# Optimization experiments

Measured on AMD Instinct MI355X. Metric: run time of the kernel, lower is better.

Reference implementation:

```python
import jax, jax.numpy as jnp
import numpy as np
from jax import lax

COEF = 0.97  # rnn.weight_hh_l0; weight_ih_l0 == 1.0


def setup_inputs() -> dict:
    key = jax.random.key(0)
    B, C, T = 128, 1, 262144
    x = jax.random.normal(key, (B, C, T), dtype=jnp.float32)
    return {"input": x}


def reference(input) -> jnp.ndarray:
    # torch.nn.RNN(1,1,1,bias=False) with weight_ih=1, weight_hh=COEF and
    # default nonlinearity='tanh':  h[t] = tanh(x[t] + COEF * h[t-1])
    x = input[:, 0, :]                     # [B, T]
    B = x.shape[0]

    def step(h, x_t):                      # h: [B], x_t: [B]
        h = jnp.tanh(x_t + COEF * h)
        return h, h

    h0 = jnp.zeros((B,), dtype=x.dtype)
    _, ys = lax.scan(step, h0, x.T)        # ys: [T, B]
    return ys.T[:, None, :]                # [B, 1, T]
```

## Files before the change

kernel.cpp:

```cpp
#include <hip/hip_runtime.h>


#define BB 128
#define TT 262144
#define CH 64
#define SPW 64
#define NBLK (BB * (TT / CH) / SPW)

typedef float f32x4 __attribute__((ext_vector_type(4)));

__global__ __launch_bounds__(64) void ipe_kernel(const float* __restrict__ x,
                                                 float* __restrict__ y) {
    const int lane = threadIdx.x;
    const int bid = (blockIdx.x & 7) * (NBLK >> 3) + (blockIdx.x >> 3);
    const int row = bid >> 6;
    const int g   = bid & 63;
    const size_t rowBase = (size_t)row * TT;
    const long   tileT0  = (long)g * (SPW * CH) - CH;

    __shared__ float tile[65 * 64];

    const int h4 = lane >> 4;
    const int t4 = lane & 15;

    f32x4 pf[17];
    #pragma unroll
    for (int m = 0; m < 16; ++m) {
        const long T = tileT0 + (long)(m * 64 + lane) * 4;
        if (T >= 0) pf[m] = *reinterpret_cast<const f32x4*>(x + rowBase + T);
        else        pf[m] = (f32x4){0.f, 0.f, 0.f, 0.f};
    }
    if (lane < 16) {
        const long T = tileT0 + (long)(16 * 64 + lane) * 4;
        pf[16] = *reinterpret_cast<const f32x4*>(x + rowBase + T);
    }

    #pragma unroll
    for (int m = 0; m < 16; ++m) {
        const int span = 4 * m + h4;
        *reinterpret_cast<f32x4*>(&tile[span * 64 + 4 * (t4 ^ (span & 15))]) = pf[m];
    }
    if (lane < 16) {
        *reinterpret_cast<f32x4*>(&tile[64 * 64 + 4 * lane]) = pf[16];
    }
    asm volatile("" ::: "memory");

    const float C2 = 2.885390081777926815f;
    const float K2 = 0.97f * C2;
    float h = 0.f;
    float xv[64];

    #pragma unroll
    for (int e = 0; e < 16; ++e) {
        f32x4 v = *reinterpret_cast<const f32x4*>(
            &tile[lane * 64 + 4 * (e ^ (lane & 15))]);
        xv[4 * e + 0] = v.x; xv[4 * e + 1] = v.y;
        xv[4 * e + 2] = v.z; xv[4 * e + 3] = v.w;
    }
    #pragma unroll
    for (int k = 0; k < 64; ++k) {
        float z2 = fmaf(K2, h, xv[k] * C2);
        float ez = __builtin_amdgcn_exp2f(z2);
        float rc = __builtin_amdgcn_rcpf(ez + 1.0f);
        h = fmaf(-2.0f, rc, 1.0f);
    }

    const int sp1 = lane + 1;
    #pragma unroll
    for (int e = 0; e < 16; ++e) {
        f32x4 v = *reinterpret_cast<const f32x4*>(
            &tile[sp1 * 64 + 4 * (e ^ (sp1 & 15))]);
        xv[4 * e + 0] = v.x; xv[4 * e + 1] = v.y;
        xv[4 * e + 2] = v.z; xv[4 * e + 3] = v.w;
    }
    #pragma unroll
    for (int k = 0; k < 64; ++k) {
        float z2 = fmaf(K2, h, xv[k] * C2);
        float ez = __builtin_amdgcn_exp2f(z2);
        float rc = __builtin_amdgcn_rcpf(ez + 1.0f);
        h = fmaf(-2.0f, rc, 1.0f);
        xv[k] = h;
    }

    asm volatile("" ::: "memory");
    #pragma unroll
    for (int e = 0; e < 16; ++e) {
        f32x4 v;
        v.x = xv[4 * e + 0]; v.y = xv[4 * e + 1];
        v.z = xv[4 * e + 2]; v.w = xv[4 * e + 3];
        *reinterpret_cast<f32x4*>(&tile[sp1 * 64 + 4 * (e ^ (sp1 & 15))]) = v;
    }
    asm volatile("" ::: "memory");

    const long outT0 = tileT0 + CH;
    #pragma unroll
    for (int m = 0; m < 16; ++m) {
        const int span = 1 + 4 * m + h4;
        f32x4 v = *reinterpret_cast<const f32x4*>(
            &tile[span * 64 + 4 * (t4 ^ (span & 15))]);
        *reinterpret_cast<f32x4*>(y + rowBase + outT0 + (long)(m * 64 + lane) * 4) = v;
    }
}

extern "C" void kernel_launch(void* const* d_in, const int* in_sizes, int n_in,
                              void* d_out, int out_size, void* d_ws, size_t ws_size,
                              hipStream_t stream) {
    const float* x = (const float*)d_in[0];
    float* y = (float*)d_out;
    ipe_kernel<<<dim3(NBLK), dim3(64), 0, stream>>>(x, y);
}
```

Before: 46.84 us.

## Shrink per-lane chunk to 32 with 64-step warmup window, two waves per block

Each lane now handles 32 outputs instead of 64. Before those, it runs a 64-step warmup recurrence over the preceding inputs (its previous two chunks) so the tanh recurrence converges, replacing the earlier 64-step warmup plus 64-step output layout. Blocks now hold two independent 64-lane waves, each with its own smaller LDS tile and a new XOR swizzle. The aim is to cut the serial dependency chain per lane from 128 to 96 steps, at the cost of a higher warmup-to-output ratio and more total transcendental work. Accuracy now relies on the 0.97 decay over 64 steps being enough, as before.

```diff
diff --git a/kernel.cpp b/kernel.cpp
--- a/kernel.cpp
+++ b/kernel.cpp
@@ -3,78 +3,91 @@
 
 #define BB 128
 #define TT 262144
-#define CH 64
-#define SPW 64
-#define NBLK (BB * (TT / CH) / SPW)
+#define CHL 32
+#define WW 64
+#define WPR 128
+#define NBLK ((BB * WPR) / 2)
 
 typedef float f32x4 __attribute__((ext_vector_type(4)));
 
-__global__ __launch_bounds__(64) void ipe_kernel(const float* __restrict__ x,
-                                                 float* __restrict__ y) {
-    const int lane = threadIdx.x;
-    const int bid = (blockIdx.x & 7) * (NBLK >> 3) + (blockIdx.x >> 3);
-    const int row = bid >> 6;
-    const int g   = bid & 63;
+__device__ __forceinline__ int swq(int q) { return q ^ ((q >> 3) & 7); }
+
+__global__ __launch_bounds__(128) void ipe_kernel(const float* __restrict__ x,
+                                                  float* __restrict__ y) {
+    const int lane = threadIdx.x & 63;
+    const int wv   = threadIdx.x >> 6;
+    const int bid  = (blockIdx.x & 7) * (NBLK >> 3) + (blockIdx.x >> 3);
+    const int w    = bid * 2 + wv;
+    const int row  = w >> 7;
+    const int g    = w & (WPR - 1);
     const size_t rowBase = (size_t)row * TT;
-    const long   tileT0  = (long)g * (SPW * CH) - CH;
+    const long   t0 = (long)g * (64 * CHL);
 
-    __shared__ float tile[65 * 64];
+    __shared__ float tile_all[2][528 * 4];
+    float* tile = tile_all[wv];
 
-    const int h4 = lane >> 4;
-    const int t4 = lane & 15;
-
-    f32x4 pf[17];
+    f32x4 pf[8], ph;
     #pragma unroll
-    for (int m = 0; m < 16; ++m) {
-        const long T = tileT0 + (long)(m * 64 + lane) * 4;
-        if (T >= 0) pf[m] = *reinterpret_cast<const f32x4*>(x + rowBase + T);
-        else        pf[m] = (f32x4){0.f, 0.f, 0.f, 0.f};
-    }
+    for (int m = 0; m < 8; ++m)
+        pf[m] = *reinterpret_cast<const f32x4*>(x + rowBase + t0 + 256 * m + 4 * lane);
     if (lane < 16) {
-        const long T = tileT0 + (long)(16 * 64 + lane) * 4;
-        pf[16] = *reinterpret_cast<const f32x4*>(x + rowBase + T);
+        const long T = t0 - WW + 4 * lane;
+        if (T >= 0) ph = *reinterpret_cast<const f32x4*>(x + rowBase + T);
+        else        ph = (f32x4){0.f, 0.f, 0.f, 0.f};
     }
 
     #pragma unroll
-    for (int m = 0; m < 16; ++m) {
-        const int span = 4 * m + h4;
-        *reinterpret_cast<f32x4*>(&tile[span * 64 + 4 * (t4 ^ (span & 15))]) = pf[m];
+    for (int m = 0; m < 8; ++m)
+        *reinterpret_cast<f32x4*>(&tile[4 * swq(16 + 64 * m + lane)]) = pf[m];
+    if (lane < 16)
+        *reinterpret_cast<f32x4*>(&tile[4 * swq(lane)]) = ph;
+    asm volatile("" ::: "memory");
+
+    float xv[32];
+    #pragma unroll
+    for (int t = 0; t < 8; ++t) {
+        f32x4 v = *reinterpret_cast<const f32x4*>(&tile[4 * swq(8 * lane + t)]);
+        xv[4 * t + 0] = v.x; xv[4 * t + 1] = v.y;
+        xv[4 * t + 2] = v.z; xv[4 * t + 3] = v.w;
     }
-    if (lane < 16) {
-        *reinterpret_cast<f32x4*>(&tile[64 * 64 + 4 * lane]) = pf[16];
-    }
-    asm volatile("" ::: "memory");
+    #pragma unroll
+    for (int t = 0; t < 8; ++t)
+        pf[t] = *reinterpret_cast<const f32x4*>(&tile[4 * swq(8 * lane + 8 + t)]);
 
     const float C2 = 2.885390081777926815f;
     const float K2 = 0.97f * C2;
     float h = 0.f;
-    float xv[64];
 
     #pragma unroll
-    for (int e = 0; e < 16; ++e) {
-        f32x4 v = *reinterpret_cast<const f32x4*>(
-            &tile[lane * 64 + 4 * (e ^ (lane & 15))]);
-        xv[4 * e + 0] = v.x; xv[4 * e + 1] = v.y;
-        xv[4 * e + 2] = v.z; xv[4 * e + 3] = v.w;
-    }
-    #pragma unroll
-    for (int k = 0; k < 64; ++k) {
+    for (int k = 0; k < 32; ++k) {
         float z2 = fmaf(K2, h, xv[k] * C2);
         float ez = __builtin_amdgcn_exp2f(z2);
         float rc = __builtin_amdgcn_rcpf(ez + 1.0f);
         h = fmaf(-2.0f, rc, 1.0f);
     }
 
-    const int sp1 = lane + 1;
     #pragma unroll
-    for (int e = 0; e < 16; ++e) {
-        f32x4 v = *reinterpret_cast<const f32x4*>(
-            &tile[sp1 * 64 + 4 * (e ^ (sp1 & 15))]);
-        xv[4 * e + 0] = v.x; xv[4 * e + 1] = v.y;
-        xv[4 * e + 2] = v.z; xv[4 * e + 3] = v.w;
+    for (int t = 0; t < 8; ++t) {
+        f32x4 v = *reinterpret_cast<const f32x4*>(&tile[4 * swq(16 + 8 * lane + t)]);
+        xv[4 * t + 0] = v.x; xv[4 * t + 1] = v.y;
+        xv[4 * t + 2] = v.z; xv[4 * t + 3] = v.w;
     }
+
     #pragma unroll
-    for (int k = 0; k < 64; ++k) {
+    for (int t = 0; t < 8; ++t) {
+        float z2, ez, rc;
+        z2 = fmaf(K2, h, pf[t].x * C2); ez = __builtin_amdgcn_exp2f(z2);
+        rc = __builtin_amdgcn_rcpf(ez + 1.0f); h = fmaf(-2.0f, rc, 1.0f);
+        z2 = fmaf(K2, h, pf[t].y * C2); ez = __builtin_amdgcn_exp2f(z2);
+        rc = __builtin_amdgcn_rcpf(ez + 1.0f); h = fmaf(-2.0f, rc, 1.0f);
+        z2 = fmaf(K2, h, pf[t].z * C2); ez = __builtin_amdgcn_exp2f(z2);
+        rc = __builtin_amdgcn_rcpf(ez + 1.0f); h = fmaf(-2.0f, rc, 1.0f);
+        z2 = fmaf(K2, h, pf[t].w * C2); ez = __builtin_amdgcn_exp2f(z2);
+        rc = __builtin_amdgcn_rcpf(ez + 1.0f); h = fmaf(-2.0f, rc, 1.0f);
+    }
+
+    #pragma unroll
+    for (int k = 0; k < 32; ++k) {
         float z2 = fmaf(K2, h, xv[k] * C2);
         float ez = __builtin_amdgcn_exp2f(z2);
         float rc = __builtin_amdgcn_rcpf(ez + 1.0f);
@@ -84,21 +97,18 @@
 
     asm volatile("" ::: "memory");
     #pragma unroll
-    for (int e = 0; e < 16; ++e) {
+    for (int t = 0; t < 8; ++t) {
         f32x4 v;
-        v.x = xv[4 * e + 0]; v.y = xv[4 * e + 1];
-        v.z = xv[4 * e + 2]; v.w = xv[4 * e + 3];
-        *reinterpret_cast<f32x4*>(&tile[sp1 * 64 + 4 * (e ^ (sp1 & 15))]) = v;
+        v.x = xv[4 * t + 0]; v.y = xv[4 * t + 1];
+        v.z = xv[4 * t + 2]; v.w = xv[4 * t + 3];
+        *reinterpret_cast<f32x4*>(&tile[4 * swq(16 + 8 * lane + t)]) = v;
     }
     asm volatile("" ::: "memory");
 
-    const long outT0 = tileT0 + CH;
     #pragma unroll
-    for (int m = 0; m < 16; ++m) {
-        const int span = 1 + 4 * m + h4;
-        f32x4 v = *reinterpret_cast<const f32x4*>(
-            &tile[span * 64 + 4 * (t4 ^ (span & 15))]);
-        *reinterpret_cast<f32x4*>(y + rowBase + outT0 + (long)(m * 64 + lane) * 4) = v;
+    for (int m = 0; m < 8; ++m) {
+        f32x4 v = *reinterpret_cast<const f32x4*>(&tile[4 * swq(16 + 64 * m + lane)]);
+        *reinterpret_cast<f32x4*>(y + rowBase + t0 + 256 * m + 4 * lane) = v;
     }
 }
 
@@ -107,5 +117,5 @@
                               hipStream_t stream) {
     const float* x = (const float*)d_in[0];
     float* y = (float*)d_out;
-    ipe_kernel<<<dim3(NBLK), dim3(64), 0, stream>>>(x, y);
+    ipe_kernel<<<dim3(NBLK), dim3(128), 0, stream>>>(x, y);
 }
```

Measured after the change: 46.22 us, median of 2. Within noise of the previous version (-1.3%).
